# Kernel optimization log

Measured on AMD Instinct MI355X. Metric: run time of the kernel, lower is better.

Reference implementation:

```python
import jax, jax.numpy as jnp
import numpy as np
from jax import lax

# ConvTranspose2d(stride=1, padding=p) == conv with spatially-flipped, in/out-swapped
# weight and padding k-1-p per side. Here k=3, p=1 -> conv padding (1,1).
K = 3
P = 1
_CONV_PAD = K - 1 - P  # = 1

def _rconv(a, w):
    # a: [N,C,H,Wf] real, w: [O,I,kH,kW]
    return lax.conv_general_dilated(
        a, w, window_strides=(1, 1),
        padding=[(_CONV_PAD, _CONV_PAD), (_CONV_PAD, _CONV_PAD)],
        dimension_numbers=("NCHW", "OIHW", "NCHW"))


def setup_inputs() -> dict:
    key = jax.random.key(0)
    k1, k2, k3, k4, k5 = jax.random.split(key, 5)
    N, C_IN, C_OUT, H, W = 8, 16, 16, 512, 512
    x = jax.random.normal(k1, (N, C_IN, H, W), dtype=jnp.float32)
    # torch ConvTranspose2d weight layout: (in, out, kH, kW), complex64 split into re/im
    scale = 1.0 / np.sqrt(C_IN * K * K)
    w_real = jax.random.normal(k2, (C_IN, C_OUT, K, K), dtype=jnp.float32) * scale
    w_imag = jax.random.normal(k3, (C_IN, C_OUT, K, K), dtype=jnp.float32) * scale
    b_real = jax.random.normal(k4, (C_OUT,), dtype=jnp.float32) * scale
    b_imag = jax.random.normal(k5, (C_OUT,), dtype=jnp.float32) * scale
    return {"x": x, "w_real": w_real, "w_imag": w_imag, "b_real": b_real, "b_imag": b_imag}


def reference(x, w_real, w_imag, b_real, b_imag):
    # rfftn over last two dims (norm='backward')
    X = jnp.fft.rfftn(x, axes=(-2, -1), norm="backward")  # [N,C,H,W//2+1] complex64
    Xr, Xi = jnp.real(X), jnp.imag(X)
    # convert transpose-conv weight to equivalent conv weight: flip spatial, swap in/out
    wr = jnp.transpose(jnp.flip(w_real, axis=(-2, -1)), (1, 0, 2, 3))
    wi = jnp.transpose(jnp.flip(w_imag, axis=(-2, -1)), (1, 0, 2, 3))
    # complex conv via real/imag decomposition
    Yr = _rconv(Xr, wr) - _rconv(Xi, wi) + b_real[:, None, None]
    Yi = _rconv(Xr, wi) + _rconv(Xi, wr) + b_imag[:, None, None]
    Y = lax.complex(Yr, Yi)
    # irfftn with no explicit s: last dim -> 2*(Wf-1) = W
    return jnp.fft.irfftn(Y, axes=(-2, -1), norm="backward")
```

## Files before the change

### kernel.cpp

```cpp
#include <hip/hip_runtime.h>
#include <math.h>

#define PI_F 3.14159265358979323846f

#define FI(i) ((i) + ((i) >> 4))
#define CSTRIDE 544
#define TSTRIDE 546

__device__ inline float2 cmulf(float2 a, float2 b) {
    return make_float2(a.x * b.x - a.y * b.y, a.x * b.y + a.y * b.x);
}
__device__ inline float2 cadd(float2 a, float2 b) { return make_float2(a.x + b.x, a.y + b.y); }
__device__ inline float2 csub(float2 a, float2 b) { return make_float2(a.x - b.x, a.y - b.y); }

__device__ inline void cmac(float2& a, float2 w, float2 v) {
    a.x = fmaf(w.x, v.x, a.x);
    a.x = fmaf(-w.y, v.y, a.x);
    a.y = fmaf(w.x, v.y, a.y);
    a.y = fmaf(w.y, v.x, a.y);
}

__device__ inline int xcd_remap(int bid, int q) {
    return (bid & 7) * q + (bid >> 3);
}

__device__ inline void build_tbl128(float2* tbl, int tid) {
    if (tid < 128) {
        float ang = -2.0f * PI_F * (float)tid * (1.0f / 512.0f);
        tbl[tid] = make_float2(cosf(ang), sinf(ang));
    }
}

template <int NCOLS>
__device__ inline float2* fft512_r4(float2* a, float2* b, const float2* tbl, int tid, bool inv) {
    const int bf = tid & 127;
    const int cp = tid >> 7;
#pragma unroll
    for (int st = 0; st < 4; ++st) {
        const int slog = 2 * st;
        const int s = 1 << slog;
        const int p = bf >> slog;
        const int q = bf & (s - 1);
        float2 w1 = tbl[p << slog];
        if (inv) w1.y = -w1.y;
        const float2 w2 = cmulf(w1, w1);
        const float2 w3 = cmulf(w2, w1);
        const int i0 = bf;
        const int ob = q + (p << (slog + 2));
#pragma unroll
        for (int t = 0; t < NCOLS / 2; ++t) {
            const int cc = cp + 2 * t;
            const float2* ac = a + cc * CSTRIDE;
            float2* bc = b + cc * CSTRIDE;
            float2 A = ac[FI(i0)];
            float2 B = ac[FI(i0 + 128)];
            float2 C = ac[FI(i0 + 256)];
            float2 D = ac[FI(i0 + 384)];
            float2 apc = cadd(A, C), amc = csub(A, C);
            float2 bpd = cadd(B, D), bmd = csub(B, D);
            float2 jb = make_float2(-bmd.y, bmd.x);
            if (inv) { jb.x = -jb.x; jb.y = -jb.y; }
            bc[FI(ob)]           = cadd(apc, bpd);
            bc[FI(ob + s)]       = cmulf(csub(amc, jb), w1);
            bc[FI(ob + 2 * s)]   = cmulf(csub(apc, bpd), w2);
            bc[FI(ob + 3 * s)]   = cmulf(cadd(amc, jb), w3);
        }
        __syncthreads();
        float2* tmp = a; a = b; b = tmp;
    }
    {
#pragma unroll
        for (int cc = 0; cc < NCOLS; ++cc) {
            const float2* ac = a + cc * CSTRIDE;
            float2* bc = b + cc * CSTRIDE;
            float2 A = ac[FI(tid)];
            float2 B = ac[FI(tid + 256)];
            bc[FI(tid)]       = cadd(A, B);
            bc[FI(tid + 256)] = csub(A, B);
        }
        __syncthreads();
        float2* tmp = a; a = b; b = tmp;
    }
    return a;
}

__device__ inline void wave_fence() {
    asm volatile("s_waitcnt lgkmcnt(0)" ::: "memory");
    __builtin_amdgcn_sched_barrier(0);
}

template <bool INV>
__device__ inline float2 rot90(float2 z) {
    return INV ? make_float2(-z.y, z.x) : make_float2(z.y, -z.x);
}

template <bool INV>
__device__ inline void dft8(float2 v[8]) {
    const float R2 = 0.70710678118654752f;
    float2 t0 = cadd(v[0], v[4]), t1 = csub(v[0], v[4]);
    float2 t2 = cadd(v[2], v[6]), t3 = csub(v[2], v[6]);
    float2 s0 = cadd(v[1], v[5]), s1 = csub(v[1], v[5]);
    float2 s2 = cadd(v[3], v[7]), s3 = csub(v[3], v[7]);
    float2 rt3 = rot90<INV>(t3), rs3 = rot90<INV>(s3);
    float2 E0 = cadd(t0, t2), E1 = cadd(t1, rt3), E2 = csub(t0, t2), E3 = csub(t1, rt3);
    float2 O0 = cadd(s0, s2), O1 = cadd(s1, rs3), O2 = csub(s0, s2), O3 = csub(s1, rs3);
    float2 rO1 = rot90<INV>(O1), rO2 = rot90<INV>(O2), rO3 = rot90<INV>(O3);
    float2 a1 = make_float2(R2 * (O1.x + rO1.x), R2 * (O1.y + rO1.y));
    float2 a2 = rO2;
    float2 a3 = make_float2(R2 * (rO3.x - O3.x), R2 * (rO3.y - O3.y));
    v[0] = cadd(E0, O0); v[4] = csub(E0, O0);
    v[1] = cadd(E1, a1); v[5] = csub(E1, a1);
    v[2] = cadd(E2, a2); v[6] = csub(E2, a2);
    v[3] = cadd(E3, a3); v[7] = csub(E3, a3);
}

__device__ inline void twiddle8(float2 v[8], float2 w1) {
    float2 w2 = cmulf(w1, w1);
    float2 w3 = cmulf(w2, w1);
    float2 w4 = cmulf(w2, w2);
    float2 w5 = cmulf(w4, w1);
    float2 w6 = cmulf(w3, w3);
    float2 w7 = cmulf(w4, w3);
    v[1] = cmulf(v[1], w1); v[2] = cmulf(v[2], w2); v[3] = cmulf(v[3], w3);
    v[4] = cmulf(v[4], w4); v[5] = cmulf(v[5], w5); v[6] = cmulf(v[6], w6);
    v[7] = cmulf(v[7], w7);
}

template <bool INV>
__device__ inline void fft512_wave_ip(float2 v[8], float2* R, int lane) {
    const float sg = INV ? (6.2831853071795865f / 512.0f)
                         : (-6.2831853071795865f / 512.0f);
    float2 w1;
    __sincosf(sg * (float)lane, &w1.y, &w1.x);
    dft8<INV>(v);
    twiddle8(v, w1);
#pragma unroll
    for (int m = 0; m < 8; ++m) R[FI(8 * lane + m)] = v[m];
    wave_fence();
#pragma unroll
    for (int j = 0; j < 8; ++j) v[j] = R[FI(lane + 64 * j)];
    float2 w1b;
    w1b.x = __shfl(w1.x, lane & 56);
    w1b.y = __shfl(w1.y, lane & 56);
    dft8<INV>(v);
    twiddle8(v, w1b);
    {
        int ob = (lane & 7) + ((lane >> 3) << 6);
#pragma unroll
        for (int m = 0; m < 8; ++m) R[FI(ob + 8 * m)] = v[m];
    }
    wave_fence();
#pragma unroll
    for (int j = 0; j < 8; ++j) v[j] = R[FI(lane + 64 * j)];
    dft8<INV>(v);
}

__global__ __launch_bounds__(256) void k_row_rfft(const float* __restrict__ x,
                                                  float2* __restrict__ G) {
    __shared__ float2 lds[4][544];
    int lane = threadIdx.x & 63;
    int w = threadIdx.x >> 6;
    int pair = blockIdx.x * 4 + w;
    const float* x0 = x + (size_t)(2 * pair) * 512;
    const float* x1 = x0 + 512;
    float2 v[8];
#pragma unroll
    for (int j = 0; j < 8; ++j)
        v[j] = make_float2(x0[lane + 64 * j], x1[lane + 64 * j]);
    fft512_wave_ip<false>(v, lds[w], lane);
    float2 P[5];
#pragma unroll
    for (int m = 0; m < 5; ++m) {
        int src = (64 - lane) & 63;
        float2 p;
        p.x = __shfl(v[7 - m].x, src);
        p.y = __shfl(v[7 - m].y, src);
        if (lane == 0) p = v[(8 - m) & 7];
        P[m] = p;
    }
    float2* g0 = G + (size_t)(2 * pair) * 257;
    float2* g1 = g0 + 257;
#pragma unroll
    for (int m = 0; m < 4; ++m) {
        int k = lane + 64 * m;
        float2 Z = v[m], Pc = P[m];
        float2 S = make_float2(0.5f * (Z.x + Pc.x), 0.5f * (Z.y - Pc.y));
        float2 D = make_float2(Z.x - Pc.x, Z.y + Pc.y);
        float2 T = make_float2(0.5f * D.y, -0.5f * D.x);
        g0[k] = S;
        g1[k] = T;
    }
    if (lane == 0) {
        float2 Z = v[4], Pc = P[4];
        g0[256] = make_float2(0.5f * (Z.x + Pc.x), 0.5f * (Z.y - Pc.y));
        float2 D = make_float2(Z.x - Pc.x, Z.y + Pc.y);
        g1[256] = make_float2(0.5f * D.y, -0.5f * D.x);
    }
}

__global__ __launch_bounds__(1024) void k_col_fft(const float2* __restrict__ G,
                                                  float2* __restrict__ XT) {
    __shared__ float2 tile[16][TSTRIDE];
    int tid = threadIdx.x;
    int l = xcd_remap(blockIdx.x, 272);
    int nc = l / 17;
    int v0 = (l % 17) * 16;
#pragma unroll
    for (int j = 0; j < 8; ++j) {
        int e = tid + 1024 * j;
        int dv = e & 15, h = e >> 4;
        int v = v0 + dv;
        float2 val = make_float2(0.0f, 0.0f);
        if (v < 257) val = G[((size_t)nc * 512 + h) * 257 + v];
        tile[dv][FI(h)] = val;
    }
    __syncthreads();
    int lane = tid & 63, w = tid >> 6;
    float2* R = tile[w];
    float2 vv[8];
#pragma unroll
    for (int j = 0; j < 8; ++j) vv[j] = R[FI(lane + 64 * j)];
    fft512_wave_ip<false>(vv, R, lane);
    int v = v0 + w;
    if (v < 257) {
        float2* dst = XT + ((size_t)nc * 257 + v) * 512;
#pragma unroll
        for (int m = 0; m < 8; ++m) dst[lane + 64 * m] = vv[m];
    }
}

__global__ __launch_bounds__(256, 4) void k_conv(const float2* __restrict__ XT,
                                                 float2* __restrict__ YT,
                                                 const float* __restrict__ wr,
                                                 const float* __restrict__ wi,
                                                 const float* __restrict__ br,
                                                 const float* __restrict__ bi) {
    __shared__ float2 Xs[16 * 4 * 66];
    int tid = threadIdx.x;
    int bid = blockIdx.x;
    int ut = bid & 7;
    int rest = bid >> 3;
    int vt = rest % 129;
    int n = rest / 129;
    int u0 = ut * 64;
    int v0 = vt * 2;

    for (int l = tid; l < 4224; l += 256) {
        int c = l / 264;
        int rem = l - c * 264;
        int dvr = rem / 66;
        int uu = rem - dvr * 66;
        int vg = v0 - 1 + dvr;
        int ug = u0 - 1 + uu;
        float2 val = make_float2(0.0f, 0.0f);
        if (vg >= 0 && vg < 257 && ug >= 0 && ug < 512)
            val = XT[(((size_t)n * 16 + c) * 257 + vg) * 512 + ug];
        Xs[l] = val;
    }
    __syncthreads();

    int lane = tid & 63;
    int wv = __builtin_amdgcn_readfirstlane(tid >> 6);
    int o0 = wv * 4;

    float2 acc[2][4];
#pragma unroll
    for (int oo = 0; oo < 4; ++oo) {
        float2 bv = make_float2(br[o0 + oo], bi[o0 + oo]);
        acc[0][oo] = bv;
        acc[1][oo] = bv;
    }

    for (int c = 0; c < 16; ++c) {
        float2 xv[4][3];
#pragma unroll
        for (int dvr = 0; dvr < 4; ++dvr) {
            const float2* row = &Xs[(c * 4 + dvr) * 66];
            xv[dvr][0] = row[lane];
            xv[dvr][1] = row[lane + 1];
            xv[dvr][2] = row[lane + 2];
        }
#pragma unroll
        for (int oo = 0; oo < 4; ++oo) {
            const float* wrp = wr + ((size_t)(c * 16 + o0 + oo)) * 9;
            const float* wip = wi + ((size_t)(c * 16 + o0 + oo)) * 9;
            float wre[9], wim[9];
#pragma unroll
            for (int t = 0; t < 9; ++t) { wre[t] = wrp[t]; wim[t] = wip[t]; }
#pragma unroll
            for (int kw = 0; kw < 3; ++kw) {
#pragma unroll
                for (int kh = 0; kh < 3; ++kh) {
                    int t = kh * 3 + kw;
                    int xj = 2 - kh;
                    float2 w = make_float2(wre[t], wim[t]);
                    cmac(acc[0][oo], w, xv[2 - kw][xj]);
                    cmac(acc[1][oo], w, xv[3 - kw][xj]);
                }
            }
        }
    }

#pragma unroll
    for (int oo = 0; oo < 4; ++oo) {
#pragma unroll
        for (int vv = 0; vv < 2; ++vv) {
            int v = v0 + vv;
            if (v < 257)
                YT[(((size_t)n * 16 + o0 + oo) * 257 + v) * 512 + u0 + lane] =
                    acc[vv][oo];
        }
    }
}

__global__ __launch_bounds__(256) void k_col_ifft(const float2* __restrict__ YT,
                                                  float2* __restrict__ ZT) {
    __shared__ float2 b0[4 * CSTRIDE], b1[4 * CSTRIDE], tbl[128];
    int tid = threadIdx.x;
    int no = blockIdx.x / 65;
    int v0 = (blockIdx.x % 65) * 4;
    build_tbl128(tbl, tid);
#pragma unroll
    for (int k = 0; k < 4; ++k) {
        int v = v0 + k;
        const float2* src = YT + ((size_t)no * 257 + (v < 257 ? v : 256)) * 512;
        b0[k * CSTRIDE + FI(tid)]       = src[tid];
        b0[k * CSTRIDE + FI(tid + 256)] = src[tid + 256];
    }
    __syncthreads();
    float2* res = fft512_r4<4>(b0, b1, tbl, tid, true);
    const float sc = 1.0f / 512.0f;
#pragma unroll
    for (int k = 0; k < 4; ++k) {
        int v = v0 + k;
        if (v < 257) {
            float2* dst = ZT + ((size_t)no * 257 + v) * 512;
            float2 r0 = res[k * CSTRIDE + FI(tid)];
            float2 r1 = res[k * CSTRIDE + FI(tid + 256)];
            dst[tid]       = make_float2(r0.x * sc, r0.y * sc);
            dst[tid + 256] = make_float2(r1.x * sc, r1.y * sc);
        }
    }
}

__global__ __launch_bounds__(512) void k_row_irfft(const float2* __restrict__ ZT,
                                                   float* __restrict__ out) {
    __shared__ float2 tile[16][TSTRIDE];
    int tid = threadIdx.x;
    int no = blockIdx.x >> 5;
    int h0 = (blockIdx.x & 31) * 16;
#pragma unroll
    for (int j = 0; j < 9; ++j) {
        int e = tid + 512 * j;
        if (e < 4112) {
            int dh = e & 15, vv = e >> 4;
            tile[dh][FI(vv)] = ZT[((size_t)no * 257 + vv) * 512 + h0 + dh];
        }
    }
    __syncthreads();
    int lane = tid & 63, w = tid >> 6;
    float2* Ra = tile[2 * w];
    float2* Rb = tile[2 * w + 1];
    float2 v[8];
#pragma unroll
    for (int m = 0; m < 8; ++m) {
        int i = lane + 64 * m;
        float2 a, b, W;
        if (i <= 256) {
            a = Ra[FI(i)];
            b = Rb[FI(i)];
            if (i == 0 || i == 256) { a.y = 0.0f; b.y = 0.0f; }
            W = make_float2(a.x - b.y, a.y + b.x);
        } else {
            int ii = 512 - i;
            a = Ra[FI(ii)];
            b = Rb[FI(ii)];
            W = make_float2(a.x + b.y, -a.y + b.x);
        }
        v[m] = W;
    }
    fft512_wave_ip<true>(v, Ra, lane);
    const float sc = 1.0f / 512.0f;
    float* d0 = out + ((size_t)no * 512 + h0 + 2 * w) * 512;
    float* d1 = d0 + 512;
#pragma unroll
    for (int m = 0; m < 8; ++m) {
        d0[lane + 64 * m] = v[m].x * sc;
        d1[lane + 64 * m] = v[m].y * sc;
    }
}

extern "C" void kernel_launch(void* const* d_in, const int* in_sizes, int n_in,
                              void* d_out, int out_size, void* d_ws, size_t ws_size,
                              hipStream_t stream) {
    const float* x  = (const float*)d_in[0];
    const float* wr = (const float*)d_in[1];
    const float* wi = (const float*)d_in[2];
    const float* br = (const float*)d_in[3];
    const float* bi = (const float*)d_in[4];
    float* out = (float*)d_out;

    const size_t bufElems = (size_t)128 * 257 * 512;
    float2* A = (float2*)d_ws;
    float2* B = A + bufElems;

    k_row_rfft<<<8192, 256, 0, stream>>>(x, A);
    k_col_fft<<<128 * 17, 1024, 0, stream>>>(A, B);
    k_conv<<<8 * 129 * 8, 256, 0, stream>>>(B, A, wr, wi, br, bi);
    k_col_ifft<<<128 * 65, 256, 0, stream>>>(A, B);
    k_row_irfft<<<128 * 32, 512, 0, stream>>>(B, out);
}
```

Before: 615.9 us.

## Use per-wave in-register FFT for column IFFT and halve conv LDS tile

The column inverse FFT drops the block-wide radix-4 shared-memory FFT, which needed five syncthreads and two ping-pong buffers. Each wave now runs a register-resident 512-point FFT on its own column with a small private LDS scratch, reusing the routine already used in the forward pass, and the last partial block's waves return early. The conv kernel loads its input channels in two halves of eight, halving its LDS footprint and raising the launch-bounds occupancy hint from 4 to 8. The cost is one extra block barrier in the conv and possibly more register pressure under the tighter occupancy target.

```diff
diff --git a/kernel.cpp b/kernel.cpp
--- a/kernel.cpp
+++ b/kernel.cpp
@@ -4,7 +4,6 @@
 #define PI_F 3.14159265358979323846f
 
 #define FI(i) ((i) + ((i) >> 4))
-#define CSTRIDE 544
 #define TSTRIDE 546
 
 __device__ inline float2 cmulf(float2 a, float2 b) {
@@ -22,66 +21,6 @@
 
 __device__ inline int xcd_remap(int bid, int q) {
     return (bid & 7) * q + (bid >> 3);
-}
-
-__device__ inline void build_tbl128(float2* tbl, int tid) {
-    if (tid < 128) {
-        float ang = -2.0f * PI_F * (float)tid * (1.0f / 512.0f);
-        tbl[tid] = make_float2(cosf(ang), sinf(ang));
-    }
-}
-
-template <int NCOLS>
-__device__ inline float2* fft512_r4(float2* a, float2* b, const float2* tbl, int tid, bool inv) {
-    const int bf = tid & 127;
-    const int cp = tid >> 7;
-#pragma unroll
-    for (int st = 0; st < 4; ++st) {
-        const int slog = 2 * st;
-        const int s = 1 << slog;
-        const int p = bf >> slog;
-        const int q = bf & (s - 1);
-        float2 w1 = tbl[p << slog];
-        if (inv) w1.y = -w1.y;
-        const float2 w2 = cmulf(w1, w1);
-        const float2 w3 = cmulf(w2, w1);
-        const int i0 = bf;
-        const int ob = q + (p << (slog + 2));
-#pragma unroll
-        for (int t = 0; t < NCOLS / 2; ++t) {
-            const int cc = cp + 2 * t;
-            const float2* ac = a + cc * CSTRIDE;
-            float2* bc = b + cc * CSTRIDE;
-            float2 A = ac[FI(i0)];
-            float2 B = ac[FI(i0 + 128)];
-            float2 C = ac[FI(i0 + 256)];
-            float2 D = ac[FI(i0 + 384)];
-            float2 apc = cadd(A, C), amc = csub(A, C);
-            float2 bpd = cadd(B, D), bmd = csub(B, D);
-            float2 jb = make_float2(-bmd.y, bmd.x);
-            if (inv) { jb.x = -jb.x; jb.y = -jb.y; }
-            bc[FI(ob)]           = cadd(apc, bpd);
-            bc[FI(ob + s)]       = cmulf(csub(amc, jb), w1);
-            bc[FI(ob + 2 * s)]   = cmulf(csub(apc, bpd), w2);
-            bc[FI(ob + 3 * s)]   = cmulf(cadd(amc, jb), w3);
-        }
-        __syncthreads();
-        float2* tmp = a; a = b; b = tmp;
-    }
-    {
-#pragma unroll
-        for (int cc = 0; cc < NCOLS; ++cc) {
-            const float2* ac = a + cc * CSTRIDE;
-            float2* bc = b + cc * CSTRIDE;
-            float2 A = ac[FI(tid)];
-            float2 B = ac[FI(tid + 256)];
-            bc[FI(tid)]       = cadd(A, B);
-            bc[FI(tid + 256)] = csub(A, B);
-        }
-        __syncthreads();
-        float2* tmp = a; a = b; b = tmp;
-    }
-    return a;
 }
 
 __device__ inline void wave_fence() {
@@ -229,13 +168,13 @@
     }
 }
 
-__global__ __launch_bounds__(256, 4) void k_conv(const float2* __restrict__ XT,
+__global__ __launch_bounds__(256, 8) void k_conv(const float2* __restrict__ XT,
                                                  float2* __restrict__ YT,
                                                  const float* __restrict__ wr,
                                                  const float* __restrict__ wi,
                                                  const float* __restrict__ br,
                                                  const float* __restrict__ bi) {
-    __shared__ float2 Xs[16 * 4 * 66];
+    __shared__ float2 Xs[8 * 4 * 66];
     int tid = threadIdx.x;
     int bid = blockIdx.x;
     int ut = bid & 7;
@@ -245,20 +184,6 @@
     int u0 = ut * 64;
     int v0 = vt * 2;
 
-    for (int l = tid; l < 4224; l += 256) {
-        int c = l / 264;
-        int rem = l - c * 264;
-        int dvr = rem / 66;
-        int uu = rem - dvr * 66;
-        int vg = v0 - 1 + dvr;
-        int ug = u0 - 1 + uu;
-        float2 val = make_float2(0.0f, 0.0f);
-        if (vg >= 0 && vg < 257 && ug >= 0 && ug < 512)
-            val = XT[(((size_t)n * 16 + c) * 257 + vg) * 512 + ug];
-        Xs[l] = val;
-    }
-    __syncthreads();
-
     int lane = tid & 63;
     int wv = __builtin_amdgcn_readfirstlane(tid >> 6);
     int o0 = wv * 4;
@@ -271,31 +196,50 @@
         acc[1][oo] = bv;
     }
 
-    for (int c = 0; c < 16; ++c) {
-        float2 xv[4][3];
-#pragma unroll
-        for (int dvr = 0; dvr < 4; ++dvr) {
-            const float2* row = &Xs[(c * 4 + dvr) * 66];
-            xv[dvr][0] = row[lane];
-            xv[dvr][1] = row[lane + 1];
-            xv[dvr][2] = row[lane + 2];
-        }
-#pragma unroll
-        for (int oo = 0; oo < 4; ++oo) {
-            const float* wrp = wr + ((size_t)(c * 16 + o0 + oo)) * 9;
-            const float* wip = wi + ((size_t)(c * 16 + o0 + oo)) * 9;
-            float wre[9], wim[9];
-#pragma unroll
-            for (int t = 0; t < 9; ++t) { wre[t] = wrp[t]; wim[t] = wip[t]; }
-#pragma unroll
-            for (int kw = 0; kw < 3; ++kw) {
-#pragma unroll
-                for (int kh = 0; kh < 3; ++kh) {
-                    int t = kh * 3 + kw;
-                    int xj = 2 - kh;
-                    float2 w = make_float2(wre[t], wim[t]);
-                    cmac(acc[0][oo], w, xv[2 - kw][xj]);
-                    cmac(acc[1][oo], w, xv[3 - kw][xj]);
+    for (int half = 0; half < 2; ++half) {
+        if (half) __syncthreads();
+        for (int l = tid; l < 2112; l += 256) {
+            int c = l / 264;
+            int rem = l - c * 264;
+            int dvr = rem / 66;
+            int uu = rem - dvr * 66;
+            int vg = v0 - 1 + dvr;
+            int ug = u0 - 1 + uu;
+            int cg = half * 8 + c;
+            float2 val = make_float2(0.0f, 0.0f);
+            if (vg >= 0 && vg < 257 && ug >= 0 && ug < 512)
+                val = XT[(((size_t)n * 16 + cg) * 257 + vg) * 512 + ug];
+            Xs[l] = val;
+        }
+        __syncthreads();
+
+        for (int c = 0; c < 8; ++c) {
+            int cg = half * 8 + c;
+            float2 xv[4][3];
+#pragma unroll
+            for (int dvr = 0; dvr < 4; ++dvr) {
+                const float2* row = &Xs[(c * 4 + dvr) * 66];
+                xv[dvr][0] = row[lane];
+                xv[dvr][1] = row[lane + 1];
+                xv[dvr][2] = row[lane + 2];
+            }
+#pragma unroll
+            for (int oo = 0; oo < 4; ++oo) {
+                const float* wrp = wr + ((size_t)(cg * 16 + o0 + oo)) * 9;
+                const float* wip = wi + ((size_t)(cg * 16 + o0 + oo)) * 9;
+                float wre[9], wim[9];
+#pragma unroll
+                for (int t = 0; t < 9; ++t) { wre[t] = wrp[t]; wim[t] = wip[t]; }
+#pragma unroll
+                for (int kw = 0; kw < 3; ++kw) {
+#pragma unroll
+                    for (int kh = 0; kh < 3; ++kh) {
+                        int t = kh * 3 + kw;
+                        int xj = 2 - kh;
+                        float2 w = make_float2(wre[t], wim[t]);
+                        cmac(acc[0][oo], w, xv[2 - kw][xj]);
+                        cmac(acc[1][oo], w, xv[3 - kw][xj]);
+                    }
                 }
             }
         }
@@ -315,32 +259,22 @@
 
 __global__ __launch_bounds__(256) void k_col_ifft(const float2* __restrict__ YT,
                                                   float2* __restrict__ ZT) {
-    __shared__ float2 b0[4 * CSTRIDE], b1[4 * CSTRIDE], tbl[128];
-    int tid = threadIdx.x;
+    __shared__ float2 lds[4][544];
+    int lane = threadIdx.x & 63;
+    int w = threadIdx.x >> 6;
     int no = blockIdx.x / 65;
-    int v0 = (blockIdx.x % 65) * 4;
-    build_tbl128(tbl, tid);
-#pragma unroll
-    for (int k = 0; k < 4; ++k) {
-        int v = v0 + k;
-        const float2* src = YT + ((size_t)no * 257 + (v < 257 ? v : 256)) * 512;
-        b0[k * CSTRIDE + FI(tid)]       = src[tid];
-        b0[k * CSTRIDE + FI(tid + 256)] = src[tid + 256];
-    }
-    __syncthreads();
-    float2* res = fft512_r4<4>(b0, b1, tbl, tid, true);
+    int v = (blockIdx.x % 65) * 4 + w;
+    if (v >= 257) return;
+    const float2* src = YT + ((size_t)no * 257 + v) * 512;
+    float2 vv[8];
+#pragma unroll
+    for (int j = 0; j < 8; ++j) vv[j] = src[lane + 64 * j];
+    fft512_wave_ip<true>(vv, lds[w], lane);
     const float sc = 1.0f / 512.0f;
-#pragma unroll
-    for (int k = 0; k < 4; ++k) {
-        int v = v0 + k;
-        if (v < 257) {
-            float2* dst = ZT + ((size_t)no * 257 + v) * 512;
-            float2 r0 = res[k * CSTRIDE + FI(tid)];
-            float2 r1 = res[k * CSTRIDE + FI(tid + 256)];
-            dst[tid]       = make_float2(r0.x * sc, r0.y * sc);
-            dst[tid + 256] = make_float2(r1.x * sc, r1.y * sc);
-        }
-    }
+    float2* dst = ZT + ((size_t)no * 257 + v) * 512;
+#pragma unroll
+    for (int m = 0; m < 8; ++m)
+        dst[lane + 64 * m] = make_float2(vv[m].x * sc, vv[m].y * sc);
 }
 
 __global__ __launch_bounds__(512) void k_row_irfft(const float2* __restrict__ ZT,
```

Result: faster. 593.4 us (-3.6%).
